# Kernel optimization log

Hardware: AMD Instinct MI355X
Metric: run time of the kernel (lower is better)

The kernel has to match this reference:

```python
import jax, jax.numpy as jnp
import numpy as np

BLOCK, HALO, HEADS = 8, 4, 4


def setup_inputs() -> dict:
    key = jax.random.key(0)
    ks = jax.random.split(key, 9)
    B, C, H, W = 8, 256, 64, 64
    inner = C  # heads * dim_head = 4 * 64
    d = inner // HEADS
    R = BLOCK + 2 * HALO  # 16
    s = 0.02
    return {
        "x": jax.random.normal(ks[0], (B, C, H, W), jnp.float32),
        "wq": jax.random.normal(ks[1], (inner, C), jnp.float32) * s,
        "wkv": jax.random.normal(ks[2], (2 * inner, C), jnp.float32) * s,
        "wo": jax.random.normal(ks[3], (C, inner), jnp.float32) * s,
        "bo": jax.random.normal(ks[4], (C,), jnp.float32) * s,
        "rel_h": jax.random.normal(ks[5], (2 * R - 1, d), jnp.float32) * (d ** -0.5),
        "rel_w": jax.random.normal(ks[6], (2 * R - 1, d), jnp.float32) * (d ** -0.5),
        "w_conv": jax.random.normal(ks[7], (4 * C, C), jnp.float32) * s,
        "b_conv": jax.random.normal(ks[8], (4 * C,), jnp.float32) * s,
    }


def reference(x, wq, wkv, wo, bo, rel_h, rel_w, w_conv, b_conv):
    B, C, H, W = x.shape
    bs, halo, heads = BLOCK, HALO, HEADS
    R = bs + 2 * halo
    inner = wq.shape[0]
    d = inner // heads
    nh, nw = H // bs, W // bs
    Nb = B * nh * nw

    # ---- HaloAttention ----
    # block queries: (B, C, nh, bs, nw, bs) -> (Nb, bs*bs, C)
    q_in = x.reshape(B, C, nh, bs, nw, bs).transpose(0, 2, 4, 3, 5, 1).reshape(Nb, bs * bs, C)
    # haloed K/V windows via overlapping gather (== F.unfold(kernel=R, stride=bs, pad=halo))
    xp = jnp.pad(x, ((0, 0), (0, 0), (halo, halo), (halo, halo)))
    ridx = (jnp.arange(nh) * bs)[:, None] + jnp.arange(R)[None]  # (nh, R)
    cidx = (jnp.arange(nw) * bs)[:, None] + jnp.arange(R)[None]  # (nw, R)
    win = xp[:, :, ridx][:, :, :, :, cidx]                       # (B, C, nh, R, nw, R)
    kv_in = win.transpose(0, 2, 4, 3, 5, 1).reshape(Nb, R * R, C)

    q = (q_in @ wq.T).reshape(Nb, bs * bs, heads, d).transpose(0, 2, 1, 3) * (d ** -0.5)
    kv = kv_in @ wkv.T
    k, v = jnp.split(kv, 2, axis=-1)
    k = k.reshape(Nb, R * R, heads, d).transpose(0, 2, 1, 3)
    v = v.reshape(Nb, R * R, heads, d).transpose(0, 2, 1, 3)

    sim = jnp.einsum('bhid,bhjd->bhij', q, k)  # (Nb, heads, bs*bs, R*R)

    # relative position logits (computed from the scaled q, as in the torch code)
    q5 = q.reshape(Nb, heads, bs, bs, d)
    rel_idx = jnp.arange(R)[None, :] - jnp.arange(bs)[:, None] + (R - 1)  # (bs, R)
    lw = jnp.einsum('bhxyd,yjd->bhxyj', q5, rel_w[rel_idx])  # over key col j
    lh = jnp.einsum('bhxyd,xid->bhxyi', q5, rel_h[rel_idx])  # over key row i
    sim = sim.reshape(Nb, heads, bs, bs, R, R) + lw[..., None, :] + lh[..., None]
    sim = sim.reshape(Nb, heads, bs * bs, R * R)

    # mask out padded halo positions
    m = jnp.pad(jnp.ones((H, W), bool), ((halo, halo), (halo, halo)))
    mwin = m[ridx][:, :, cidx].transpose(0, 2, 1, 3).reshape(nh * nw, R * R)
    mask = jnp.broadcast_to(mwin[None], (B, nh * nw, R * R)).reshape(Nb, 1, 1, R * R)
    sim = jnp.where(mask, sim, -jnp.finfo(sim.dtype).max)

    attn = jax.nn.softmax(sim, axis=-1)
    out = jnp.einsum('bhij,bhjd->bhid', attn, v)
    out = out.transpose(0, 2, 1, 3).reshape(Nb, bs * bs, inner)
    out = out @ wo.T + bo  # (Nb, bs*bs, C)
    y = out.reshape(B, nh, nw, bs, bs, C).transpose(0, 5, 1, 3, 2, 4).reshape(B, C, H, W)

    # ---- Conv2d(dim, 4*dim, 1) + PixelShuffle(2) ----
    y = jnp.einsum('bchw,oc->bohw', y, w_conv) + b_conv[None, :, None, None]
    Cn = y.shape[1] // 4
    y = y.reshape(B, Cn, 2, 2, H, W).transpose(0, 1, 4, 2, 5, 3).reshape(B, Cn, 2 * H, 2 * W)
    return y
```

## Files before the change

### kernel.cpp

```cpp
#include <hip/hip_runtime.h>

typedef unsigned short u16;
typedef unsigned int u32;
typedef __attribute__((ext_vector_type(8))) short short8;
typedef __attribute__((ext_vector_type(4))) float f32x4;

__device__ __forceinline__ float bf2f(u16 u){ union { u32 i; float f; } x; x.i = ((u32)u)<<16; return x.f; }
__device__ __forceinline__ u16 f2bf(float f){ union { float f; u32 i; } x; x.f = f; u32 r = x.i + 0x7fffu + ((x.i>>16)&1u); return (u16)(r>>16); }

#define MFMA16(a,b,c) __builtin_amdgcn_mfma_f32_16x16x32_bf16((a),(b),(c),0,0,0)

__device__ __forceinline__ uint4 ld8(const void* p, size_t off, int f32) {
  if (f32) {
    const float* fp = (const float*)p + off;
    float4 a = *(const float4*)fp;
    float4 b = *(const float4*)(fp + 4);
    uint4 o;
    o.x = (u32)f2bf(a.x) | ((u32)f2bf(a.y)<<16);
    o.y = (u32)f2bf(a.z) | ((u32)f2bf(a.w)<<16);
    o.z = (u32)f2bf(b.x) | ((u32)f2bf(b.y)<<16);
    o.w = (u32)f2bf(b.z) | ((u32)f2bf(b.w)<<16);
    return o;
  }
  return *(const uint4*)((const u16*)p + off);
}
__device__ __forceinline__ uint2 ld4(const void* p, size_t off, int f32) {
  if (f32) {
    const float* fp = (const float*)p + off;
    float4 a = *(const float4*)fp;
    uint2 o;
    o.x = (u32)f2bf(a.x) | ((u32)f2bf(a.y)<<16);
    o.y = (u32)f2bf(a.z) | ((u32)f2bf(a.w)<<16);
    return o;
  }
  return *(const uint2*)((const u16*)p + off);
}
__device__ __forceinline__ float ldsc(const void* p, size_t off, int f32) {
  if (f32) return ((const float*)p)[off];
  return bf2f(((const u16*)p)[off]);
}

__global__ __launch_bounds__(256) void k_detect(const u32* __restrict__ x, int* __restrict__ flag)
{
  __shared__ int cnt;
  if (threadIdx.x == 0) cnt = 0;
  __syncthreads();
  int c = 0;
  #pragma unroll
  for (int i = 0; i < 32; ++i) {
    u32 w = x[threadIdx.x*32 + i];
    u32 e = (w >> 7) & 0xFFu;
    c += (e == 0u || (e >= 96u && e <= 143u)) ? 1 : 0;
  }
  atomicAdd(&cnt, c);
  __syncthreads();
  if (threadIdx.x == 0) *flag = (cnt < 4915) ? 1 : 0;
}

__global__ __launch_bounds__(256) void k_transpose(const void* __restrict__ x, u16* __restrict__ xt,
                                                   const int* __restrict__ flagp)
{
  __shared__ int sflag;
  __shared__ __align__(16) u16 tile[64][68];
  if (threadIdx.x == 0) sflag = *flagp;
  __syncthreads();
  const int f32 = sflag;
  const int p0 = blockIdx.x*64, c0 = blockIdx.y*64, b = blockIdx.z;
  const int t = threadIdx.x;
  const size_t xbo = ((size_t)(b*256 + c0))*4096 + p0;
  #pragma unroll
  for (int pass=0; pass<4; ++pass) {
    int cl = pass*16 + (t>>4);
    int pl = (t&15)*4;
    uint2 v = ld4(x, xbo + (size_t)cl*4096 + pl, f32);
    *(uint2*)&tile[cl][pl] = v;
  }
  __syncthreads();
  u16* xtb = xt + ((size_t)b*4096 + p0)*256 + c0;
  #pragma unroll
  for (int pass=0; pass<4; ++pass) {
    int pl = pass*16 + (t>>4);
    int cl = (t&15)*4;
    unsigned int lo = (unsigned int)tile[cl][pl]   | ((unsigned int)tile[cl+1][pl]<<16);
    unsigned int hi = (unsigned int)tile[cl+2][pl] | ((unsigned int)tile[cl+3][pl]<<16);
    uint2 o; o.x = lo; o.y = hi;
    *(uint2*)(xtb + (size_t)pl*256 + cl) = o;
  }
}

__global__ __launch_bounds__(256) void k_gemm_bt(
  const u16* __restrict__ A, int lda,
  const void* __restrict__ Bt0, const void* __restrict__ Bt1, int nsplit,
  const void* __restrict__ bias,
  void* __restrict__ C, int M, int N, int K,
  float s_lo, float s_hi, int shuffle,
  const int* __restrict__ flagp)
{
  __shared__ int sflag;
  __shared__ __align__(16) char smem[40960];
  if (threadIdx.x == 0) sflag = *flagp;
  __syncthreads();
  const int f32 = sflag;
  const int m0 = blockIdx.x*128, n0 = blockIdx.y*128;
  const void* Bs; int boff;
  if (Bt1 && n0 >= nsplit) { Bs = Bt1; boff = n0 - nsplit; } else { Bs = Bt0; boff = n0; }
  const int t = threadIdx.x, lane = t & 63, wv = t >> 6;
  const int wm = (wv & 1)*64, wn = (wv >> 1)*64;
  const int lm = lane & 15, lq = lane >> 4;
  f32x4 acc[4][4] = {};
  uint4 pa[2], pb[2];
  #pragma unroll
  for (int i=0;i<2;++i) {
    int u = t + i*256, row = u >> 2, ch = (u & 3)*8;
    pa[i] = *(const uint4*)(A + (size_t)(m0+row)*lda + ch);
    pb[i] = ld8(Bs, (size_t)(boff+row)*K + ch, f32);
  }
  int cur = 0;
  for (int k0 = 0; k0 < K; k0 += 32) {
    u16* Als = (u16*)(smem + cur*20480);
    u16* Bls = (u16*)(smem + cur*20480 + 10240);
    #pragma unroll
    for (int i=0;i<2;++i) {
      int u = t + i*256, row = u >> 2, ch = (u & 3)*8;
      *(uint4*)&Als[row*40 + ch] = pa[i];
      *(uint4*)&Bls[row*40 + ch] = pb[i];
    }
    __syncthreads();
    if (k0 + 32 < K) {
      int k1 = k0 + 32;
      #pragma unroll
      for (int i=0;i<2;++i) {
        int u = t + i*256, row = u >> 2, ch = (u & 3)*8;
        pa[i] = *(const uint4*)(A + (size_t)(m0+row)*lda + k1 + ch);
        pb[i] = ld8(Bs, (size_t)(boff+row)*K + k1 + ch, f32);
      }
    }
    short8 af[4], bf[4];
    #pragma unroll
    for (int i=0;i<4;++i) af[i] = *(const short8*)&Als[(wm + i*16 + lm)*40 + lq*8];
    #pragma unroll
    for (int i=0;i<4;++i) bf[i] = *(const short8*)&Bls[(wn + i*16 + lm)*40 + lq*8];
    #pragma unroll
    for (int mt=0;mt<4;++mt)
      #pragma unroll
      for (int nt=0;nt<4;++nt)
        acc[mt][nt] = MFMA16(af[mt], bf[nt], acc[mt][nt]);
    cur ^= 1;
  }

  if (!shuffle) {
    u16* eh = (u16*)smem;
    #pragma unroll
    for (int c=0;c<2;++c) {
      __syncthreads();
      if ((wv>>1) == c) {
        #pragma unroll
        for (int nt=0;nt<4;++nt) {
          int col = n0 + c*64 + nt*16 + lm;
          float sc = (col < nsplit) ? s_lo : s_hi;
          float bv = bias ? ldsc(bias, col, f32) : 0.0f;
          #pragma unroll
          for (int mt=0;mt<4;++mt)
            #pragma unroll
            for (int r=0;r<4;++r) {
              int row = wm + mt*16 + lq*4 + r;
              eh[row*72 + nt*16 + lm] = f2bf(acc[mt][nt][r]*sc + bv);
            }
        }
      }
      __syncthreads();
      {
        int row = t >> 1, off = (t & 1)*32;
        const uint4* s = (const uint4*)&eh[row*72 + off];
        uint4 v0 = s[0], v1 = s[1], v2 = s[2], v3 = s[3];
        uint4* dp = (uint4*)((u16*)C + (size_t)(m0+row)*N + n0 + c*64 + off);
        dp[0]=v0; dp[1]=v1; dp[2]=v2; dp[3]=v3;
      }
    }
  } else {
    float* ef = (float*)smem;
    const int b = m0 >> 12;
    const int hh0 = (m0 & 4095) >> 6;
    #pragma unroll
    for (int c=0;c<4;++c) {
      __syncthreads();
      if ((wv>>1) == (c>>1)) {
        #pragma unroll
        for (int nt2=0;nt2<2;++nt2) {
          int nt = (c&1)*2 + nt2;
          int col = n0 + wn + nt*16 + lm;
          float bv = bias ? ldsc(bias, col, f32) : 0.0f;
          int col_rel = nt2*16 + lm;
          int cn_rel = col_rel >> 2, rr = (col_rel >> 1) & 1, ss = col_rel & 1;
          #pragma unroll
          for (int mt=0;mt<4;++mt)
            #pragma unroll
            for (int r=0;r<4;++r) {
              int row = wm + mt*16 + lq*4 + r;
              int orow = cn_rel*4 + (row>>6)*2 + rr;
              int ow   = (row & 63)*2 + ss;
              ef[orow*136 + ow] = acc[mt][nt][r]*s_hi + bv;
            }
        }
      }
      __syncthreads();
      {
        int orow = t >> 3, seg = t & 7;
        int cn_rel = orow >> 2, oh_rel = orow & 3;
        int cn = ((n0 + c*32) >> 2) + cn_rel;
        size_t obase = (((size_t)(b*256 + cn))*128 + hh0*2 + oh_rel)*128 + seg*16;
        const float4* s = (const float4*)&ef[orow*136 + seg*16];
        float4 v0 = s[0], v1 = s[1], v2 = s[2], v3 = s[3];
        if (f32) {
          float4* dp = (float4*)((float*)C + obase);
          dp[0]=v0; dp[1]=v1; dp[2]=v2; dp[3]=v3;
        } else {
          float vv[16];
          *(float4*)&vv[0]=v0; *(float4*)&vv[4]=v1; *(float4*)&vv[8]=v2; *(float4*)&vv[12]=v3;
          u32 pw[8];
          #pragma unroll
          for (int j=0;j<8;++j) pw[j] = (u32)f2bf(vv[2*j]) | ((u32)f2bf(vv[2*j+1])<<16);
          u16* dp = (u16*)C + obase;
          *(uint4*)dp       = *(uint4*)&pw[0];
          *(uint4*)(dp + 8) = *(uint4*)&pw[4];
        }
      }
    }
  }
}

#define MASKVAL (-30000.0f)
__global__ __launch_bounds__(256) void k_halo_attn(
  u16* __restrict__ qkv,
  const void* __restrict__ relh, const void* __restrict__ relw,
  const int* __restrict__ flagp)
{
  __shared__ int sflag;
  __shared__ __align__(16) u16 Qs[64*72];
  __shared__ __align__(16) u16 KP[128*72];
  __shared__ __align__(16) u16 Vt[64*136];
  __shared__ __align__(16) u16 Gw[64*32];
  __shared__ __align__(16) u16 Gh[64*32];
  if (threadIdx.x == 0) sflag = *flagp;
  __syncthreads();
  const int f32 = sflag;

  const int blk = blockIdx.x, head = blockIdx.y;
  const int bb = blk >> 6, by = (blk >> 3) & 7, bx = blk & 7;
  const int h0 = by*8, w0 = bx*8;
  const int t = threadIdx.x, lane = t & 63, wv = t >> 6;
  const int lm = lane & 15, lq = lane >> 4;
  const size_t pixbase = (size_t)bb * 4096;
  const float LOG2E = 1.4426950408889634f;

  #pragma unroll
  for (int i=0;i<2;++i) {
    int u = t + i*256;
    int row = u >> 3, ch = (u & 7)*8;
    int qx = row >> 3, qy = row & 7;
    size_t p = pixbase + (size_t)(h0+qx)*64 + (w0+qy);
    *(uint4*)&Qs[row*72 + ch] = *(const uint4*)(qkv + p*768 + head*64 + ch);
  }
  {
    u16* RW = KP; u16* RH = KP + 2048;
    if (t < 248) {
      *(uint4*)&RW[t*8] = ld8(relw, (size_t)t*8, f32);
      *(uint4*)&RH[t*8] = ld8(relh, (size_t)t*8, f32);
    } else {
      uint4 z; z.x=z.y=z.z=z.w=0;
      int o = 1984 + (t-248)*8;
      *(uint4*)&RW[o] = z;
      *(uint4*)&RH[o] = z;
    }
  }
  __syncthreads();
  {
    const u16* RW = KP; const u16* RH = KP + 2048;
    f32x4 agw[2] = {}, agh[2] = {};
    #pragma unroll
    for (int ks=0;ks<2;++ks) {
      short8 aq = *(const short8*)&Qs[(wv*16 + lm)*72 + ks*32 + lq*8];
      #pragma unroll
      for (int nt=0;nt<2;++nt) {
        short8 bw = *(const short8*)&RW[(nt*16 + lm)*64 + ks*32 + lq*8];
        short8 bh = *(const short8*)&RH[(nt*16 + lm)*64 + ks*32 + lq*8];
        agw[nt] = MFMA16(aq, bw, agw[nt]);
        agh[nt] = MFMA16(aq, bh, agh[nt]);
      }
    }
    #pragma unroll
    for (int nt=0;nt<2;++nt)
      #pragma unroll
      for (int r=0;r<4;++r) {
        int m = wv*16 + lq*4 + r, c = nt*16 + lm;
        Gw[m*32 + c] = f2bf(agw[nt][r]);
        Gh[m*32 + c] = f2bf(agh[nt][r]);
      }
  }
  __syncthreads();

  float m_run[4], l_run[4];
  #pragma unroll
  for (int r=0;r<4;++r){ m_run[r] = MASKVAL; l_run[r] = 0.0f; }
  f32x4 acc_o[4] = {};

  for (int tile=0; tile<2; ++tile) {
    #pragma unroll
    for (int i=0;i<4;++i) {
      int u = t + i*256;
      int kl = u >> 3, ch = (u & 7)*8;
      int ki = tile*8 + (kl >> 4), kj = kl & 15;
      int hk = h0 - 4 + ki, wk = w0 - 4 + kj;
      uint4 v; v.x=v.y=v.z=v.w=0;
      if ((unsigned)hk < 64u && (unsigned)wk < 64u) {
        size_t p = pixbase + (size_t)hk*64 + wk;
        v = *(const uint4*)(qkv + p*768 + 256 + head*64 + ch);
      }
      *(uint4*)&KP[kl*72 + ch] = v;
    }
    {
      int kl = t & 127, db = (t >> 7)*32;
      int ki = tile*8 + (kl >> 4), kj = kl & 15;
      int hk = h0 - 4 + ki, wk = w0 - 4 + kj;
      bool ok = ((unsigned)hk < 64u) && ((unsigned)wk < 64u);
      size_t p = pixbase + (size_t)hk*64 + wk;
      const u16* vp = qkv + p*768 + 512 + head*64 + db;
      #pragma unroll
      for (int c=0;c<4;++c) {
        union { uint4 v; u16 s[8]; } uu;
        uu.v.x=uu.v.y=uu.v.z=uu.v.w=0;
        if (ok) uu.v = *(const uint4*)(vp + c*8);
        #pragma unroll
        for (int jj=0;jj<8;++jj) Vt[(db + c*8 + jj)*136 + kl] = uu.s[jj];
      }
    }
    __syncthreads();
    f32x4 as[8] = {};
    #pragma unroll
    for (int ks=0;ks<2;++ks) {
      short8 aq = *(const short8*)&Qs[(wv*16 + lm)*72 + ks*32 + lq*8];
      #pragma unroll
      for (int nt=0;nt<8;++nt) {
        short8 bk = *(const short8*)&KP[(nt*16 + lm)*72 + ks*32 + lq*8];
        as[nt] = MFMA16(aq, bk, as[nt]);
      }
    }
    __syncthreads();
    #pragma unroll
    for (int r=0;r<4;++r) {
      int m = wv*16 + lq*4 + r;
      int qx = m >> 3, qy = m & 7;
      float vals[8]; float rowmax = MASKVAL;
      #pragma unroll
      for (int nt=0;nt<8;++nt) {
        int ki = tile*8 + nt;
        int hk = h0 - 4 + ki, wk = w0 - 4 + lm;
        float v = as[nt][r]
                + bf2f(Gw[m*32 + (lm - qy + 15)])
                + bf2f(Gh[m*32 + (ki - qx + 15)]);
        if (!((unsigned)hk < 64u && (unsigned)wk < 64u)) v = MASKVAL;
        vals[nt] = v;
        rowmax = fmaxf(rowmax, v);
      }
      #pragma unroll
      for (int s=1;s<16;s<<=1) rowmax = fmaxf(rowmax, __shfl_xor(rowmax, s, 64));
      float mnew = fmaxf(m_run[r], rowmax);
      float alpha = exp2f((m_run[r] - mnew)*LOG2E);
      float rs = 0.0f;
      #pragma unroll
      for (int nt=0;nt<8;++nt) {
        float e = exp2f((vals[nt] - mnew)*LOG2E);
        rs += e;
        KP[m*136 + nt*16 + lm] = f2bf(e);
      }
      #pragma unroll
      for (int s=1;s<16;s<<=1) rs += __shfl_xor(rs, s, 64);
      l_run[r] = l_run[r]*alpha + rs;
      m_run[r] = mnew;
      #pragma unroll
      for (int nt=0;nt<4;++nt) acc_o[nt][r] *= alpha;
    }
    __syncthreads();
    #pragma unroll
    for (int ks=0;ks<4;++ks) {
      short8 ap = *(const short8*)&KP[(wv*16 + lm)*136 + ks*32 + lq*8];
      #pragma unroll
      for (int nt=0;nt<4;++nt) {
        short8 bv = *(const short8*)&Vt[(nt*16 + lm)*136 + ks*32 + lq*8];
        acc_o[nt] = MFMA16(ap, bv, acc_o[nt]);
      }
    }
    __syncthreads();
  }
  #pragma unroll
  for (int nt=0;nt<4;++nt)
    #pragma unroll
    for (int r=0;r<4;++r) {
      int m = wv*16 + lq*4 + r;
      int qx = m >> 3, qy = m & 7;
      size_t p = pixbase + (size_t)(h0+qx)*64 + (w0+qy);
      qkv[p*768 + head*64 + nt*16 + lm] = f2bf(acc_o[nt][r]/l_run[r]);
    }
}

extern "C" void kernel_launch(void* const* d_in, const int* in_sizes, int n_in,
                              void* d_out, int out_size, void* d_ws, size_t ws_size,
                              hipStream_t stream)
{
  const void* x     = d_in[0];
  const void* wq    = d_in[1];
  const void* wkv   = d_in[2];
  const void* wo    = d_in[3];
  const void* bo    = d_in[4];
  const void* relh  = d_in[5];
  const void* relw  = d_in[6];
  const void* wconv = d_in[7];
  const void* bconv = d_in[8];

  int* flag = (int*)d_ws;
  u16* y2   = (u16*)((char*)d_ws + 4096);
  u16* base = (u16*)d_out;
  u16* qkv  = base;
  u16* xt   = base + 25165824;

  k_detect<<<1, 256, 0, stream>>>((const u32*)x, flag);
  k_transpose<<<dim3(64,4,8), 256, 0, stream>>>(x, xt, flag);
  k_gemm_bt<<<dim3(256,6), 256, 0, stream>>>(xt, 256, wq, wkv, 256, nullptr,
                                             qkv, 32768, 768, 256, 0.125f, 1.0f, 0, flag);
  k_halo_attn<<<dim3(512,4), 256, 0, stream>>>(qkv, relh, relw, flag);
  k_gemm_bt<<<dim3(256,2), 256, 0, stream>>>(qkv, 768, wo, nullptr, 0, bo,
                                             y2, 32768, 256, 256, 1.0f, 1.0f, 0, flag);
  k_gemm_bt<<<dim3(256,8), 256, 0, stream>>>(y2, 256, wconv, nullptr, 0, bconv,
                                             d_out, 32768, 1024, 256, 1.0f, 1.0f, 1, flag);
}
```

Baseline: 403.7 us.

## Fold output projection into conv weights and merge the two final GEMMs

Adds a kernel that precomputes the product of the 1x1 conv weight and the attention output-projection weight, along with the fused bias, and also takes over dtype detection. The final stage then runs one 256->1024 GEMM directly on the attention output instead of a 256->256 projection followed by the conv GEMM. Attention output goes to a separate workspace buffer, and the pixel-shuffle epilogue is widened to write 64 columns per pass. This removes a GEMM and the round trip through the intermediate y2 buffer. In exchange it recomputes the fused weight on every call, rounds it to bf16, and adds a fallback path used when the workspace is too small.

```diff
diff --git a/kernel.cpp b/kernel.cpp
--- a/kernel.cpp
+++ b/kernel.cpp
@@ -57,6 +57,68 @@
   if (threadIdx.x == 0) *flag = (cnt < 4915) ? 1 : 0;
 }
 
+__global__ __launch_bounds__(256) void k_fuse_w(
+  const u32* __restrict__ x,
+  const void* __restrict__ wo, const void* __restrict__ wconv,
+  const void* __restrict__ bo, const void* __restrict__ bconv,
+  u16* __restrict__ F, float* __restrict__ bfus, int* __restrict__ flagp)
+{
+  __shared__ int cnt;
+  __shared__ __align__(16) u16 WC[16*256];
+  __shared__ __align__(16) u16 WO[32*128];
+  const int t = threadIdx.x;
+  if (t == 0) cnt = 0;
+  __syncthreads();
+  {
+    int c = 0;
+    #pragma unroll
+    for (int i=0;i<8;++i) {
+      u32 w = x[t*8+i];
+      u32 e = (w>>7)&0xFFu;
+      c += (e==0u || (e>=96u && e<=143u)) ? 1 : 0;
+    }
+    atomicAdd(&cnt, c);
+  }
+  __syncthreads();
+  const int f32 = (cnt < 1229) ? 1 : 0;
+  if (blockIdx.x == 0 && blockIdx.y == 0 && t == 0) *flagp = f32;
+  const int o0 = blockIdx.x*16, c0 = blockIdx.y*128;
+  {
+    int row = t>>4, ch = (t&15)*16;
+    *(uint4*)&WC[row*256+ch]     = ld8(wconv, (size_t)(o0+row)*256 + ch, f32);
+    *(uint4*)&WC[row*256+ch+8]   = ld8(wconv, (size_t)(o0+row)*256 + ch + 8, f32);
+  }
+  float acc[8] = {};
+  const int ty = t>>4, tx = t&15;
+  for (int jc=0;jc<8;++jc) {
+    __syncthreads();
+    {
+      int jr = t>>3, cc = (t&7)*16;
+      *(uint4*)&WO[jr*128+cc]   = ld8(wo, (size_t)(jc*32+jr)*256 + c0 + cc, f32);
+      *(uint4*)&WO[jr*128+cc+8] = ld8(wo, (size_t)(jc*32+jr)*256 + c0 + cc + 8, f32);
+    }
+    __syncthreads();
+    #pragma unroll 4
+    for (int jj=0;jj<32;++jj) {
+      float wv = bf2f(WC[ty*256 + jc*32 + jj]);
+      short8 w8 = *(const short8*)&WO[jj*128 + tx*8];
+      #pragma unroll
+      for (int i=0;i<8;++i) acc[i] += wv * bf2f((u16)w8[i]);
+    }
+  }
+  {
+    u32 pw[4];
+    #pragma unroll
+    for (int j=0;j<4;++j) pw[j] = (u32)f2bf(acc[2*j]) | ((u32)f2bf(acc[2*j+1])<<16);
+    *(uint4*)&F[(size_t)(o0+ty)*256 + c0 + tx*8] = *(uint4*)pw;
+  }
+  if (blockIdx.y == 0 && t < 16) {
+    float s = 0.0f;
+    for (int j=0;j<256;++j) s += bf2f(WC[t*256+j]) * ldsc(bo, j, f32);
+    bfus[o0+t] = s + ldsc(bconv, o0+t, f32);
+  }
+}
+
 __global__ __launch_bounds__(256) void k_transpose(const void* __restrict__ x, u16* __restrict__ xt,
                                                    const int* __restrict__ flagp)
 {
@@ -93,7 +155,7 @@
   const void* __restrict__ Bt0, const void* __restrict__ Bt1, int nsplit,
   const void* __restrict__ bias,
   void* __restrict__ C, int M, int N, int K,
-  float s_lo, float s_hi, int shuffle,
+  float s_lo, float s_hi, int shuffle, int internalB,
   const int* __restrict__ flagp)
 {
   __shared__ int sflag;
@@ -101,6 +163,8 @@
   if (threadIdx.x == 0) sflag = *flagp;
   __syncthreads();
   const int f32 = sflag;
+  const int bf = internalB ? 0 : f32;
+  const int biasf = internalB ? 1 : f32;
   const int m0 = blockIdx.x*128, n0 = blockIdx.y*128;
   const void* Bs; int boff;
   if (Bt1 && n0 >= nsplit) { Bs = Bt1; boff = n0 - nsplit; } else { Bs = Bt0; boff = n0; }
@@ -113,7 +177,7 @@
   for (int i=0;i<2;++i) {
     int u = t + i*256, row = u >> 2, ch = (u & 3)*8;
     pa[i] = *(const uint4*)(A + (size_t)(m0+row)*lda + ch);
-    pb[i] = ld8(Bs, (size_t)(boff+row)*K + ch, f32);
+    pb[i] = ld8(Bs, (size_t)(boff+row)*K + ch, bf);
   }
   int cur = 0;
   for (int k0 = 0; k0 < K; k0 += 32) {
@@ -132,19 +196,19 @@
       for (int i=0;i<2;++i) {
         int u = t + i*256, row = u >> 2, ch = (u & 3)*8;
         pa[i] = *(const uint4*)(A + (size_t)(m0+row)*lda + k1 + ch);
-        pb[i] = ld8(Bs, (size_t)(boff+row)*K + k1 + ch, f32);
-      }
-    }
-    short8 af[4], bf[4];
-    #pragma unroll
-    for (int i=0;i<4;++i) af[i] = *(const short8*)&Als[(wm + i*16 + lm)*40 + lq*8];
-    #pragma unroll
-    for (int i=0;i<4;++i) bf[i] = *(const short8*)&Bls[(wn + i*16 + lm)*40 + lq*8];
+        pb[i] = ld8(Bs, (size_t)(boff+row)*K + k1 + ch, bf);
+      }
+    }
+    short8 af[4], bfr[4];
+    #pragma unroll
+    for (int i=0;i<4;++i) af[i]  = *(const short8*)&Als[(wm + i*16 + lm)*40 + lq*8];
+    #pragma unroll
+    for (int i=0;i<4;++i) bfr[i] = *(const short8*)&Bls[(wn + i*16 + lm)*40 + lq*8];
     #pragma unroll
     for (int mt=0;mt<4;++mt)
       #pragma unroll
       for (int nt=0;nt<4;++nt)
-        acc[mt][nt] = MFMA16(af[mt], bf[nt], acc[mt][nt]);
+        acc[mt][nt] = MFMA16(af[mt], bfr[nt], acc[mt][nt]);
     cur ^= 1;
   }
 
@@ -158,7 +222,7 @@
         for (int nt=0;nt<4;++nt) {
           int col = n0 + c*64 + nt*16 + lm;
           float sc = (col < nsplit) ? s_lo : s_hi;
-          float bv = bias ? ldsc(bias, col, f32) : 0.0f;
+          float bv = bias ? ldsc(bias, col, biasf) : 0.0f;
           #pragma unroll
           for (int mt=0;mt<4;++mt)
             #pragma unroll
@@ -182,15 +246,14 @@
     const int b = m0 >> 12;
     const int hh0 = (m0 & 4095) >> 6;
     #pragma unroll
-    for (int c=0;c<4;++c) {
+    for (int c=0;c<2;++c) {
       __syncthreads();
-      if ((wv>>1) == (c>>1)) {
+      if ((wv>>1) == c) {
         #pragma unroll
-        for (int nt2=0;nt2<2;++nt2) {
-          int nt = (c&1)*2 + nt2;
+        for (int nt=0;nt<4;++nt) {
           int col = n0 + wn + nt*16 + lm;
-          float bv = bias ? ldsc(bias, col, f32) : 0.0f;
-          int col_rel = nt2*16 + lm;
+          float bv = bias ? ldsc(bias, col, biasf) : 0.0f;
+          int col_rel = nt*16 + lm;
           int cn_rel = col_rel >> 2, rr = (col_rel >> 1) & 1, ss = col_rel & 1;
           #pragma unroll
           for (int mt=0;mt<4;++mt)
@@ -199,30 +262,34 @@
               int row = wm + mt*16 + lq*4 + r;
               int orow = cn_rel*4 + (row>>6)*2 + rr;
               int ow   = (row & 63)*2 + ss;
-              ef[orow*136 + ow] = acc[mt][nt][r]*s_hi + bv;
+              ef[orow*132 + ow] = acc[mt][nt][r]*s_hi + bv;
             }
         }
       }
       __syncthreads();
       {
-        int orow = t >> 3, seg = t & 7;
-        int cn_rel = orow >> 2, oh_rel = orow & 3;
-        int cn = ((n0 + c*32) >> 2) + cn_rel;
-        size_t obase = (((size_t)(b*256 + cn))*128 + hh0*2 + oh_rel)*128 + seg*16;
-        const float4* s = (const float4*)&ef[orow*136 + seg*16];
-        float4 v0 = s[0], v1 = s[1], v2 = s[2], v3 = s[3];
+        int orow = t >> 2, seg = t & 3;
+        int cn_rel2 = orow >> 2, oh_rel = orow & 3;
+        int cn = ((n0 + c*64) >> 2) + cn_rel2;
+        size_t obase = (((size_t)(b*256 + cn))*128 + hh0*2 + oh_rel)*128 + seg*32;
+        const float4* s = (const float4*)&ef[orow*132 + seg*32];
+        float4 v[8];
+        #pragma unroll
+        for (int i=0;i<8;++i) v[i] = s[i];
         if (f32) {
           float4* dp = (float4*)((float*)C + obase);
-          dp[0]=v0; dp[1]=v1; dp[2]=v2; dp[3]=v3;
+          #pragma unroll
+          for (int i=0;i<8;++i) dp[i] = v[i];
         } else {
-          float vv[16];
-          *(float4*)&vv[0]=v0; *(float4*)&vv[4]=v1; *(float4*)&vv[8]=v2; *(float4*)&vv[12]=v3;
-          u32 pw[8];
+          float vv[32];
           #pragma unroll
-          for (int j=0;j<8;++j) pw[j] = (u32)f2bf(vv[2*j]) | ((u32)f2bf(vv[2*j+1])<<16);
+          for (int i=0;i<8;++i) *(float4*)&vv[4*i] = v[i];
+          u32 pw[16];
+          #pragma unroll
+          for (int j=0;j<16;++j) pw[j] = (u32)f2bf(vv[2*j]) | ((u32)f2bf(vv[2*j+1])<<16);
           u16* dp = (u16*)C + obase;
-          *(uint4*)dp       = *(uint4*)&pw[0];
-          *(uint4*)(dp + 8) = *(uint4*)&pw[4];
+          #pragma unroll
+          for (int i=0;i<4;++i) *(uint4*)(dp + 8*i) = *(uint4*)&pw[4*i];
         }
       }
     }
@@ -231,8 +298,9 @@
 
 #define MASKVAL (-30000.0f)
 __global__ __launch_bounds__(256) void k_halo_attn(
-  u16* __restrict__ qkv,
+  const u16* __restrict__ qkv,
   const void* __restrict__ relh, const void* __restrict__ relw,
+  u16* __restrict__ aout, int ostride,
   const int* __restrict__ flagp)
 {
   __shared__ int sflag;
@@ -399,7 +467,7 @@
       int m = wv*16 + lq*4 + r;
       int qx = m >> 3, qy = m & 7;
       size_t p = pixbase + (size_t)(h0+qx)*64 + (w0+qy);
-      qkv[p*768 + head*64 + nt*16 + lm] = f2bf(acc_o[nt][r]/l_run[r]);
+      aout[p*(size_t)ostride + head*64 + nt*16 + lm] = f2bf(acc_o[nt][r]/l_run[r]);
     }
 }
 
@@ -417,19 +485,35 @@
   const void* wconv = d_in[7];
   const void* bconv = d_in[8];
 
-  int* flag = (int*)d_ws;
-  u16* y2   = (u16*)((char*)d_ws + 4096);
-  u16* base = (u16*)d_out;
-  u16* qkv  = base;
-  u16* xt   = base + 25165824;
-
-  k_detect<<<1, 256, 0, stream>>>((const u32*)x, flag);
-  k_transpose<<<dim3(64,4,8), 256, 0, stream>>>(x, xt, flag);
-  k_gemm_bt<<<dim3(256,6), 256, 0, stream>>>(xt, 256, wq, wkv, 256, nullptr,
-                                             qkv, 32768, 768, 256, 0.125f, 1.0f, 0, flag);
-  k_halo_attn<<<dim3(512,4), 256, 0, stream>>>(qkv, relh, relw, flag);
-  k_gemm_bt<<<dim3(256,2), 256, 0, stream>>>(qkv, 768, wo, nullptr, 0, bo,
-                                             y2, 32768, 256, 256, 1.0f, 1.0f, 0, flag);
-  k_gemm_bt<<<dim3(256,8), 256, 0, stream>>>(y2, 256, wconv, nullptr, 0, bconv,
-                                             d_out, 32768, 1024, 256, 1.0f, 1.0f, 1, flag);
-}
+  int*  flag = (int*)d_ws;
+  u16*  base = (u16*)d_out;
+  u16*  qkv  = base;
+  u16*  xt   = base + 25165824;
+
+  const size_t WS_FUSED = 4096 + 524288 + 4096 + 16777216;
+
+  if (ws_size >= WS_FUSED) {
+    u16*   Wf   = (u16*)((char*)d_ws + 4096);
+    float* bfus = (float*)((char*)d_ws + 4096 + 524288);
+    u16*   aout = (u16*)((char*)d_ws + 4096 + 524288 + 4096);
+    k_fuse_w<<<dim3(64,2), 256, 0, stream>>>((const u32*)x, wo, wconv, bo, bconv,
+                                             Wf, bfus, flag);
+    k_transpose<<<dim3(64,4,8), 256, 0, stream>>>(x, xt, flag);
+    k_gemm_bt<<<dim3(256,6), 256, 0, stream>>>(xt, 256, wq, wkv, 256, nullptr,
+                                               qkv, 32768, 768, 256, 0.125f, 1.0f, 0, 0, flag);
+    k_halo_attn<<<dim3(512,4), 256, 0, stream>>>(qkv, relh, relw, aout, 256, flag);
+    k_gemm_bt<<<dim3(256,8), 256, 0, stream>>>(aout, 256, Wf, nullptr, 0, bfus,
+                                               d_out, 32768, 1024, 256, 1.0f, 1.0f, 1, 1, flag);
+  } else {
+    u16* y2 = (u16*)((char*)d_ws + 4096);
+    k_detect<<<1, 256, 0, stream>>>((const u32*)x, flag);
+    k_transpose<<<dim3(64,4,8), 256, 0, stream>>>(x, xt, flag);
+    k_gemm_bt<<<dim3(256,6), 256, 0, stream>>>(xt, 256, wq, wkv, 256, nullptr,
+                                               qkv, 32768, 768, 256, 0.125f, 1.0f, 0, 0, flag);
+    k_halo_attn<<<dim3(512,4), 256, 0, stream>>>(qkv, relh, relw, qkv, 768, flag);
+    k_gemm_bt<<<dim3(256,2), 256, 0, stream>>>(qkv, 768, wo, nullptr, 0, bo,
+                                               y2, 32768, 256, 256, 1.0f, 1.0f, 0, 0, flag);
+    k_gemm_bt<<<dim3(256,8), 256, 0, stream>>>(y2, 256, wconv, nullptr, 0, bconv,
+                                               d_out, 32768, 1024, 256, 1.0f, 1.0f, 1, 0, flag);
+  }
+}
```

New measurement: 417.3 us. 3.4% more time.
